# Kernel optimization log

Hardware: AMD Instinct MI355X
Metric: run time of the kernel (lower is better)

## Reference

```python
import jax, jax.numpy as jnp
import numpy as np
from jax import lax

SEQ, B, F, L = 32, 32, 64, 256
OC = 128          # out_channels
K = 5
PAD = (K - 1) // 2
GROUPS = 4 * OC // 32  # GroupNorm groups = 16
EPS = 1e-5


def group_norm(x, w, b):
    # x: (B, C, L); normalize over each group's (C//G, L) slice
    bsz, c, l = x.shape
    xg = x.reshape(bsz, GROUPS, -1)
    mu = jnp.mean(xg, axis=-1, keepdims=True)
    var = jnp.var(xg, axis=-1, keepdims=True)
    xg = (xg - mu) * lax.rsqrt(var + EPS)
    return xg.reshape(bsz, c, l) * w[None, :, None] + b[None, :, None]


def setup_inputs() -> dict:
    key = jax.random.key(0)
    k1, k2, k3 = jax.random.split(key, 3)
    fan_in = (F + OC) * K
    return {
        "inputs": jax.random.normal(k1, (SEQ, B, F, L), dtype=jnp.float32),
        "conv_w": jax.random.normal(k2, (4 * OC, F + OC, K), dtype=jnp.float32) / np.sqrt(fan_in),
        "conv_b": jax.random.normal(k3, (4 * OC,), dtype=jnp.float32) * 0.01,
        "gn_w": jnp.ones((4 * OC,), dtype=jnp.float32),
        "gn_b": jnp.zeros((4 * OC,), dtype=jnp.float32),
    }


def reference(inputs, conv_w, conv_b, gn_w, gn_b):
    bsz, sub_len = inputs.shape[1], inputs.shape[3]
    hx0 = jnp.zeros((bsz, OC, sub_len), dtype=inputs.dtype)
    cx0 = jnp.zeros((bsz, OC, sub_len), dtype=inputs.dtype)

    def step(carry, x):
        hx, cx = carry
        combined = jnp.concatenate([x, hx], axis=1)  # (B, F+OC, L)
        gates = lax.conv_general_dilated(
            combined, conv_w, window_strides=(1,), padding=[(PAD, PAD)],
            dimension_numbers=("NCH", "OIH", "NCH"))
        gates = gates + conv_b[None, :, None]
        gates = group_norm(gates, gn_w, gn_b)
        i, f, g, o = jnp.split(gates, 4, axis=1)
        cy = jax.nn.sigmoid(f) * cx + jax.nn.sigmoid(i) * jnp.tanh(g)
        hy = jax.nn.sigmoid(o) * jnp.tanh(cy)
        return (hy, cy), hy

    (hy, cy), outputs = lax.scan(step, (hx0, cx0), inputs)
    return outputs, (hy, cy)
```

## Files before the change

### kernel.cpp

```cpp
#include <hip/hip_runtime.h>

typedef unsigned short u16;
typedef unsigned int u32;
typedef unsigned long long u64;
typedef __attribute__((ext_vector_type(4))) float f32x4;
typedef __attribute__((ext_vector_type(8))) short s16x8;
typedef __attribute__((ext_vector_type(4))) int i32x4;

#define EPS 1e-5f

__device__ __forceinline__ u16 f2bf(float f) {
  unsigned u = __float_as_uint(f);
  return (u16)((u + 0x7fffu + ((u >> 16) & 1u)) >> 16);
}
__device__ __forceinline__ float sigm(float x) { return 1.0f / (1.0f + __expf(-x)); }
__device__ __forceinline__ float tanh_f(float x) {
  float e = __expf(-2.0f * fabsf(x));
  float r = (1.0f - e) / (1.0f + e);
  return copysignf(r, x);
}
__device__ __forceinline__ void gl_lds16(const void* g, void* l) {
  __builtin_amdgcn_global_load_lds(
      (const __attribute__((address_space(1))) u32*)g,
      (__attribute__((address_space(3))) u32*)l, 16, 0, 0);
}

__global__ __launch_bounds__(256) void k_setup(
    const float* __restrict__ cw, u16* __restrict__ Wpk,
    const float* __restrict__ x, u16* __restrict__ xT,
    i32x4* __restrict__ hTz, i32x4* __restrict__ cxz, i32x4* __restrict__ flz) {
  const int bid = blockIdx.x, tid = threadIdx.x;
  __shared__ __align__(16) u16 ltile[256 * 72];
  if (bid < 1920) {
    int idx = bid * 256 + tid;
    int f = idx >> 9, r = idx & 511;
    int lane = r >> 3, j = r & 7;
    int of = f & 31, tk = f >> 5;
    int kk = tk % 6, tap = tk / 6;
    int o = (of << 4) + (lane & 15);
    int c = (kk << 5) + ((lane >> 4) << 3) + j;
    Wpk[idx] = f2bf(cw[(o * 192 + c) * 5 + tap]);
  } else if (bid < 2944) {
    int tb = bid - 1920;
    const float* src = x + tb * (64 * 256);
    for (int it = 0; it < 64; ++it) {
      int idx = it * 256 + tid;
      int c = idx >> 8, l = idx & 255;
      ltile[l * 72 + c] = f2bf(src[idx]);
    }
    __syncthreads();
    char* dst = (char*)(xT + tb * 16896);
    i32x4 z = {0, 0, 0, 0};
    for (int i = tid; i < 2112; i += 256) {
      int r = i >> 3, ch = i & 7;
      i32x4 v = z;
      if (r >= 2 && r < 258) v = *(const i32x4*)(ltile + (r - 2) * 72 + ch * 8);
      *(i32x4*)(dst + r * 128 + ((ch * 16) ^ ((r & 7) << 4))) = v;
    }
  } else {
    int base = (bid - 2944) * 256 + tid;
    i32x4 z = {0, 0, 0, 0};
    for (int i = base; i < 270336; i += 131072) hTz[i] = z;
    for (int i = base; i < 262144; i += 131072) cxz[i] = z;
    for (int i = base; i < 2048;   i += 131072) flz[i] = z;
  }
}

__global__ __launch_bounds__(512) void k_step(
    const u16* __restrict__ Wpk, const u16* __restrict__ xT, u16* __restrict__ hT,
    const float* __restrict__ cb, const float* __restrict__ gnw, const float* __restrict__ gnb,
    float* __restrict__ cx, float* __restrict__ out,
    float* __restrict__ stats, int* __restrict__ flags, int t) {
  const int bid = blockIdx.x;
  const int b = bid & 31, lh = (bid >> 5) & 1, cs = bid >> 6;
  const int L0 = lh << 7;
  const int tid = threadIdx.x, wave = tid >> 6, lane = tid & 63;
  const int wm = wave & 1, wl = wave >> 1;
  const int l15 = lane & 15, q = lane >> 4;
  const int cgrp = q << 4;

  __shared__ __align__(16) char ldsx[16896];
  __shared__ __align__(16) char ldsh[33792];
  __shared__ __align__(16) char hl[8192];
  __shared__ float red[8][4][2];
  __shared__ float blkstat[8];
  __shared__ float smu[4], srs[4];

  const u16* hTr = hT + (t & 1) * 1081344;
  u16* hTw = hT + ((t + 1) & 1) * 1081344;

  {
    const char* gx = (const char*)(xT + ((t << 5) + b) * 16896) + (lh << 14);
    for (int i = tid; i < 1056; i += 512) gl_lds16(gx + (i << 4), ldsx + (i << 4));
  }
  __builtin_amdgcn_sched_barrier(0);
  {
    const char* gh = (const char*)hTr + b * 67584 + (lh << 15);
    for (int i = tid; i < 2112; i += 512) gl_lds16(gh + (i << 4), ldsh + (i << 4));
  }
  __builtin_amdgcn_sched_barrier(0);
  asm volatile("s_waitcnt vmcnt(4)" ::: "memory");
  __builtin_amdgcn_s_barrier();
  __builtin_amdgcn_sched_barrier(0);

  f32x4 zero4 = {0.f, 0.f, 0.f, 0.f};
  f32x4 acc[4][2];
  #pragma unroll
  for (int g = 0; g < 4; ++g) { acc[g][0] = zero4; acc[g][1] = zero4; }

  const s16x8* Wv = (const s16x8*)Wpk;

  #pragma unroll
  for (int tap = 0; tap < 5; ++tap) {
    #pragma unroll
    for (int kk = 0; kk < 2; ++kk) {
      const int cc = tap * 6 + kk;
      s16x8 av[4], bv[2];
      #pragma unroll
      for (int g = 0; g < 4; ++g) {
        const int of = (g << 3) + (cs << 1) + wm;
        av[g] = Wv[(((cc << 5) + of) << 6) + lane];
      }
      #pragma unroll
      for (int ni = 0; ni < 2; ++ni) {
        const int rr = (wl << 5) + (ni << 4) + l15 + tap;
        const int sw = (rr & 7) << 4;
        bv[ni] = *(const s16x8*)(ldsx + (rr << 7) + (((kk << 6) + cgrp) ^ sw));
      }
      #pragma unroll
      for (int g = 0; g < 4; ++g) {
        acc[g][0] = __builtin_amdgcn_mfma_f32_16x16x32_bf16(av[g], bv[0], acc[g][0], 0, 0, 0);
        acc[g][1] = __builtin_amdgcn_mfma_f32_16x16x32_bf16(av[g], bv[1], acc[g][1], 0, 0, 0);
      }
    }
  }
  __builtin_amdgcn_sched_barrier(0);
  asm volatile("s_waitcnt vmcnt(0)" ::: "memory");
  __builtin_amdgcn_s_barrier();
  __builtin_amdgcn_sched_barrier(0);

  #pragma unroll
  for (int tap = 0; tap < 5; ++tap) {
    #pragma unroll
    for (int kk2 = 0; kk2 < 4; ++kk2) {
      const int cc = tap * 6 + kk2 + 2;
      s16x8 av[4], bv[2];
      #pragma unroll
      for (int g = 0; g < 4; ++g) {
        const int of = (g << 3) + (cs << 1) + wm;
        av[g] = Wv[(((cc << 5) + of) << 6) + lane];
      }
      #pragma unroll
      for (int ni = 0; ni < 2; ++ni) {
        const int rr = (wl << 5) + (ni << 4) + l15 + tap;
        const int sw = (rr & 7) << 4;
        bv[ni] = *(const s16x8*)(ldsh + (rr << 8) + (((kk2 << 6) + cgrp) ^ sw));
      }
      #pragma unroll
      for (int g = 0; g < 4; ++g) {
        acc[g][0] = __builtin_amdgcn_mfma_f32_16x16x32_bf16(av[g], bv[0], acc[g][0], 0, 0, 0);
        acc[g][1] = __builtin_amdgcn_mfma_f32_16x16x32_bf16(av[g], bv[1], acc[g][1], 0, 0, 0);
      }
    }
  }

  const int chq = (cs << 5) + (wm << 4) + (q << 2);
  float sum4[4], sq4[4];
  #pragma unroll
  for (int g = 0; g < 4; ++g) {
    const f32x4 bias = *(const f32x4*)(cb + (g << 7) + chq);
    sum4[g] = 0.f; sq4[g] = 0.f;
    #pragma unroll
    for (int ni = 0; ni < 2; ++ni)
      #pragma unroll
      for (int r = 0; r < 4; ++r) {
        float v = acc[g][ni][r] + bias[r];
        acc[g][ni][r] = v;
        sum4[g] += v; sq4[g] += v * v;
      }
  }
  f32x4 w4[4], b4[4];
  float cxv[2][4];
  #pragma unroll
  for (int g = 0; g < 4; ++g) {
    w4[g] = *(const f32x4*)(gnw + (g << 7) + chq);
    b4[g] = *(const f32x4*)(gnb + (g << 7) + chq);
  }
  #pragma unroll
  for (int ni = 0; ni < 2; ++ni) {
    const int l = L0 + (wl << 5) + (ni << 4) + l15;
    #pragma unroll
    for (int r = 0; r < 4; ++r)
      cxv[ni][r] = cx[(b << 15) + ((chq + r) << 8) + l];
  }
  #pragma unroll
  for (int off = 1; off < 64; off <<= 1) {
    #pragma unroll
    for (int g = 0; g < 4; ++g) {
      sum4[g] += __shfl_xor(sum4[g], off);
      sq4[g]  += __shfl_xor(sq4[g], off);
    }
  }
  if (lane == 0) {
    #pragma unroll
    for (int g = 0; g < 4; ++g) { red[wave][g][0] = sum4[g]; red[wave][g][1] = sq4[g]; }
  }
  __syncthreads();
  if (tid < 8) {
    const int g = tid >> 1, j = tid & 1;
    float v = 0.f;
    #pragma unroll
    for (int w = 0; w < 8; ++w) v += red[w][g][j];
    blkstat[tid] = v;
  }
  __syncthreads();

  const int sidx = (((t << 5) + b) << 3) + (cs << 1) + lh;
  if (tid == 0) {
    float* sp = stats + (sidx << 3);
    #pragma unroll
    for (int j = 0; j < 8; ++j)
      __hip_atomic_store(sp + j, blkstat[j], __ATOMIC_RELAXED, __HIP_MEMORY_SCOPE_AGENT);
    __hip_atomic_store(&flags[sidx], 1, __ATOMIC_RELEASE, __HIP_MEMORY_SCOPE_AGENT);
    while (__hip_atomic_load(&flags[sidx ^ 1], __ATOMIC_RELAXED, __HIP_MEMORY_SCOPE_AGENT) == 0)
      __builtin_amdgcn_s_sleep(2);
    __builtin_amdgcn_fence(__ATOMIC_ACQUIRE, "agent");
    const float* pe = stats + ((sidx & ~1) << 3);
    const float* po = stats + ((sidx | 1) << 3);
    const float inv = 1.0f / 8192.0f;
    #pragma unroll
    for (int g = 0; g < 4; ++g) {
      float s = __hip_atomic_load(pe + (g << 1), __ATOMIC_RELAXED, __HIP_MEMORY_SCOPE_AGENT)
              + __hip_atomic_load(po + (g << 1), __ATOMIC_RELAXED, __HIP_MEMORY_SCOPE_AGENT);
      float qv = __hip_atomic_load(pe + (g << 1) + 1, __ATOMIC_RELAXED, __HIP_MEMORY_SCOPE_AGENT)
               + __hip_atomic_load(po + (g << 1) + 1, __ATOMIC_RELAXED, __HIP_MEMORY_SCOPE_AGENT);
      float m = s * inv;
      smu[g] = m;
      srs[g] = rsqrtf(qv * inv - m * m + EPS);
    }
  }
  __syncthreads();

  const float mu0 = smu[0], mu1 = smu[1], mu2 = smu[2], mu3 = smu[3];
  const float rs0 = srs[0], rs1 = srs[1], rs2 = srs[2], rs3 = srs[3];
  float* outp = out + (((t << 5) + b) << 15);
  #pragma unroll
  for (int ni = 0; ni < 2; ++ni) {
    const int l = L0 + (wl << 5) + (ni << 4) + l15;
    const int ll = l - L0;
    u16 hp[4];
    #pragma unroll
    for (int r = 0; r < 4; ++r) {
      const int c = chq + r;
      float vi = (acc[0][ni][r] - mu0) * rs0 * w4[0][r] + b4[0][r];
      float vf = (acc[1][ni][r] - mu1) * rs1 * w4[1][r] + b4[1][r];
      float vg = (acc[2][ni][r] - mu2) * rs2 * w4[2][r] + b4[2][r];
      float vo = (acc[3][ni][r] - mu3) * rs3 * w4[3][r] + b4[3][r];
      float cyv = sigm(vf) * cxv[ni][r] + sigm(vi) * tanh_f(vg);
      float hyv = sigm(vo) * tanh_f(cyv);
      const int ci = (c << 8) + l;
      cx[(b << 15) + ci] = cyv;
      outp[ci] = hyv;
      hp[r] = f2bf(hyv);
      if (t == 31) {
        out[33554432 + (b << 15) + ci] = hyv;
        out[34603008 + (b << 15) + ci] = cyv;
      }
    }
    *(u64*)(hl + (ll << 6) + (((wm << 5) + (q << 3)) ^ ((ll & 3) << 4))) =
        *(const u64*)hp;
  }
  __syncthreads();

  {
    const int ll = tid >> 2, k = tid & 3;
    const int row = L0 + ll + 2;
    i32x4 v = *(const i32x4*)(hl + (ll << 6) + ((k << 4) ^ ((ll & 3) << 4)));
    char* dst = (char*)hTw + b * 67584 + (row << 8) +
                ((((cs << 2) + k) << 4) ^ ((row & 7) << 4));
    *(i32x4*)dst = v;
  }
}

extern "C" void kernel_launch(void* const* d_in, const int* in_sizes, int n_in,
                              void* d_out, int out_size, void* d_ws, size_t ws_size,
                              hipStream_t stream) {
  const float* x  = (const float*)d_in[0];
  const float* cw = (const float*)d_in[1];
  const float* cb = (const float*)d_in[2];
  const float* gw = (const float*)d_in[3];
  const float* gb = (const float*)d_in[4];
  float* out = (float*)d_out;
  char* ws = (char*)d_ws;

  u16*   Wpk   = (u16*)(ws);
  u16*   xT    = (u16*)(ws + 983040);
  u16*   hT    = (u16*)(ws + 35586048);
  float* cx    = (float*)(ws + 39911424);
  float* stats = (float*)(ws + 44105728);
  int*   flags = (int*)(ws + 44367872);

  k_setup<<<3456, 256, 0, stream>>>(cw, Wpk, x, xT, (i32x4*)hT, (i32x4*)cx, (i32x4*)flags);
  for (int t = 0; t < 32; ++t)
    k_step<<<256, 512, 0, stream>>>(Wpk, xT, hT, cb, gw, gb, cx, out, stats, flags, t);
}
```

Baseline: 665.4 us.

## Split step kernel into 512 blocks of 256 threads with four-way stat exchange

Each step kernel now runs 512 blocks of 256 threads, with each block handling a quarter of the sequence length instead of a half. This fills more of the CUs on the device and lets two blocks share a CU, at the cost of more halo reload and more cross-block GroupNorm synchronisation. The stats exchange is reworked so that eight threads store partial sums directly and three lanes each spin on one of three peer flags. Four lanes then combine the group stats. The flag buffer is moved and enlarged to fit the bigger grid.

Measured after the change: 738.2 us. 1.11x slower.

```diff
diff --git a/kernel.cpp b/kernel.cpp
--- a/kernel.cpp
+++ b/kernel.cpp
@@ -62,41 +62,40 @@
     i32x4 z = {0, 0, 0, 0};
     for (int i = base; i < 270336; i += 131072) hTz[i] = z;
     for (int i = base; i < 262144; i += 131072) cxz[i] = z;
-    for (int i = base; i < 2048;   i += 131072) flz[i] = z;
-  }
-}
-
-__global__ __launch_bounds__(512) void k_step(
+    if (base < 4096) flz[base] = z;
+  }
+}
+
+__global__ __launch_bounds__(256, 2) void k_step(
     const u16* __restrict__ Wpk, const u16* __restrict__ xT, u16* __restrict__ hT,
     const float* __restrict__ cb, const float* __restrict__ gnw, const float* __restrict__ gnb,
     float* __restrict__ cx, float* __restrict__ out,
     float* __restrict__ stats, int* __restrict__ flags, int t) {
   const int bid = blockIdx.x;
-  const int b = bid & 31, lh = (bid >> 5) & 1, cs = bid >> 6;
-  const int L0 = lh << 7;
+  const int b = bid & 31, lq = (bid >> 5) & 3, cs = bid >> 7;
+  const int L0 = lq << 6;
   const int tid = threadIdx.x, wave = tid >> 6, lane = tid & 63;
   const int wm = wave & 1, wl = wave >> 1;
   const int l15 = lane & 15, q = lane >> 4;
   const int cgrp = q << 4;
 
-  __shared__ __align__(16) char ldsx[16896];
-  __shared__ __align__(16) char ldsh[33792];
-  __shared__ __align__(16) char hl[8192];
-  __shared__ float red[8][4][2];
-  __shared__ float blkstat[8];
+  __shared__ __align__(16) char ldsx[8704];
+  __shared__ __align__(16) char ldsh[17408];
+  __shared__ __align__(16) char hl[4096];
+  __shared__ float red[4][4][2];
   __shared__ float smu[4], srs[4];
 
   const u16* hTr = hT + (t & 1) * 1081344;
   u16* hTw = hT + ((t + 1) & 1) * 1081344;
 
   {
-    const char* gx = (const char*)(xT + ((t << 5) + b) * 16896) + (lh << 14);
-    for (int i = tid; i < 1056; i += 512) gl_lds16(gx + (i << 4), ldsx + (i << 4));
+    const char* gx = (const char*)(xT + ((t << 5) + b) * 16896) + (lq << 13);
+    for (int i = tid; i < 544; i += 256) gl_lds16(gx + (i << 4), ldsx + (i << 4));
   }
   __builtin_amdgcn_sched_barrier(0);
   {
-    const char* gh = (const char*)hTr + b * 67584 + (lh << 15);
-    for (int i = tid; i < 2112; i += 512) gl_lds16(gh + (i << 4), ldsh + (i << 4));
+    const char* gh = (const char*)hTr + b * 67584 + (lq << 14);
+    for (int i = tid; i < 1088; i += 256) gl_lds16(gh + (i << 4), ldsh + (i << 4));
   }
   __builtin_amdgcn_sched_barrier(0);
   asm volatile("s_waitcnt vmcnt(4)" ::: "memory");
@@ -206,37 +205,37 @@
     for (int g = 0; g < 4; ++g) { red[wave][g][0] = sum4[g]; red[wave][g][1] = sq4[g]; }
   }
   __syncthreads();
+
+  const int gbase = ((((t << 5) + b) << 2) + cs) << 2;
+  const int sidx = gbase | lq;
   if (tid < 8) {
     const int g = tid >> 1, j = tid & 1;
-    float v = 0.f;
-    #pragma unroll
-    for (int w = 0; w < 8; ++w) v += red[w][g][j];
-    blkstat[tid] = v;
-  }
-  __syncthreads();
-
-  const int sidx = (((t << 5) + b) << 3) + (cs << 1) + lh;
-  if (tid == 0) {
-    float* sp = stats + (sidx << 3);
-    #pragma unroll
-    for (int j = 0; j < 8; ++j)
-      __hip_atomic_store(sp + j, blkstat[j], __ATOMIC_RELAXED, __HIP_MEMORY_SCOPE_AGENT);
-    __hip_atomic_store(&flags[sidx], 1, __ATOMIC_RELEASE, __HIP_MEMORY_SCOPE_AGENT);
-    while (__hip_atomic_load(&flags[sidx ^ 1], __ATOMIC_RELAXED, __HIP_MEMORY_SCOPE_AGENT) == 0)
-      __builtin_amdgcn_s_sleep(2);
-    __builtin_amdgcn_fence(__ATOMIC_ACQUIRE, "agent");
-    const float* pe = stats + ((sidx & ~1) << 3);
-    const float* po = stats + ((sidx | 1) << 3);
-    const float inv = 1.0f / 8192.0f;
-    #pragma unroll
-    for (int g = 0; g < 4; ++g) {
-      float s = __hip_atomic_load(pe + (g << 1), __ATOMIC_RELAXED, __HIP_MEMORY_SCOPE_AGENT)
-              + __hip_atomic_load(po + (g << 1), __ATOMIC_RELAXED, __HIP_MEMORY_SCOPE_AGENT);
-      float qv = __hip_atomic_load(pe + (g << 1) + 1, __ATOMIC_RELAXED, __HIP_MEMORY_SCOPE_AGENT)
-               + __hip_atomic_load(po + (g << 1) + 1, __ATOMIC_RELAXED, __HIP_MEMORY_SCOPE_AGENT);
+    float v = red[0][g][j] + red[1][g][j] + red[2][g][j] + red[3][g][j];
+    __hip_atomic_store(stats + (sidx << 3) + tid, v, __ATOMIC_RELAXED, __HIP_MEMORY_SCOPE_AGENT);
+  }
+  if (wave == 0) {
+    asm volatile("s_waitcnt vmcnt(0)" ::: "memory");
+    if (tid == 0)
+      __hip_atomic_store(&flags[sidx], 1, __ATOMIC_RELEASE, __HIP_MEMORY_SCOPE_AGENT);
+    if (tid < 3) {
+      const int p = tid + (tid >= lq ? 1 : 0);
+      while (__hip_atomic_load(&flags[gbase | p], __ATOMIC_RELAXED, __HIP_MEMORY_SCOPE_AGENT) == 0)
+        __builtin_amdgcn_s_sleep(2);
+    }
+    if (tid < 4) {
+      __builtin_amdgcn_fence(__ATOMIC_ACQUIRE, "agent");
+      float s = 0.f, qv = 0.f;
+      #pragma unroll
+      for (int p = 0; p < 4; ++p) {
+        s  += __hip_atomic_load(stats + ((gbase | p) << 3) + (tid << 1),
+                                __ATOMIC_RELAXED, __HIP_MEMORY_SCOPE_AGENT);
+        qv += __hip_atomic_load(stats + ((gbase | p) << 3) + (tid << 1) + 1,
+                                __ATOMIC_RELAXED, __HIP_MEMORY_SCOPE_AGENT);
+      }
+      const float inv = 1.0f / 8192.0f;
       float m = s * inv;
-      smu[g] = m;
-      srs[g] = rsqrtf(qv * inv - m * m + EPS);
+      smu[tid] = m;
+      srs[tid] = rsqrtf(qv * inv - m * m + EPS);
     }
   }
   __syncthreads();
@@ -298,9 +297,9 @@
   u16*   hT    = (u16*)(ws + 35586048);
   float* cx    = (float*)(ws + 39911424);
   float* stats = (float*)(ws + 44105728);
-  int*   flags = (int*)(ws + 44367872);
+  int*   flags = (int*)(ws + 44630016);
 
   k_setup<<<3456, 256, 0, stream>>>(cw, Wpk, x, xT, (i32x4*)hT, (i32x4*)cx, (i32x4*)flags);
   for (int t = 0; t < 32; ++t)
-    k_step<<<256, 512, 0, stream>>>(Wpk, xT, hT, cb, gw, gb, cx, out, stats, flags, t);
-}
+    k_step<<<512, 256, 0, stream>>>(Wpk, xT, hT, cb, gw, gb, cx, out, stats, flags, t);
+}
```

## Fuse two LSTM timesteps per launch with a per-batch inter-block flag barrier

Applied to the files above, without the earlier changes.

Each launch now runs two consecutive timesteps. Between them, the 8 blocks that share a batch element synchronize through epoch flags in global memory, then reload the new hidden state. This halves the number of kernel launches and their launch and drain overhead, and the next step's x tile is prefetched before the barrier. It relies on all 256 blocks being co-resident so the spin-waits cannot deadlock, and it adds an extra flag region that must be zeroed at setup.

New measurement: 1.561 ms. 135% more time.

```diff
diff --git a/kernel.cpp b/kernel.cpp
--- a/kernel.cpp
+++ b/kernel.cpp
@@ -62,15 +62,15 @@
     i32x4 z = {0, 0, 0, 0};
     for (int i = base; i < 270336; i += 131072) hTz[i] = z;
     for (int i = base; i < 262144; i += 131072) cxz[i] = z;
-    for (int i = base; i < 2048;   i += 131072) flz[i] = z;
+    for (int i = base; i < 3072;   i += 131072) flz[i] = z;
   }
 }
 
-__global__ __launch_bounds__(512) void k_step(
+__global__ __launch_bounds__(512, 1) void k_step2(
     const u16* __restrict__ Wpk, const u16* __restrict__ xT, u16* __restrict__ hT,
     const float* __restrict__ cb, const float* __restrict__ gnw, const float* __restrict__ gnb,
     float* __restrict__ cx, float* __restrict__ out,
-    float* __restrict__ stats, int* __restrict__ flags, int t) {
+    float* __restrict__ stats, int* __restrict__ flags, int* __restrict__ flags2, int t0) {
   const int bid = blockIdx.x;
   const int b = bid & 31, lh = (bid >> 5) & 1, cs = bid >> 6;
   const int L0 = lh << 7;
@@ -81,21 +81,17 @@
 
   __shared__ __align__(16) char ldsx[16896];
   __shared__ __align__(16) char ldsh[33792];
-  __shared__ __align__(16) char hl[8192];
+  __shared__ __align__(16) char hl[32768];
   __shared__ float red[8][4][2];
-  __shared__ float blkstat[8];
   __shared__ float smu[4], srs[4];
 
-  const u16* hTr = hT + (t & 1) * 1081344;
-  u16* hTw = hT + ((t + 1) & 1) * 1081344;
-
   {
-    const char* gx = (const char*)(xT + ((t << 5) + b) * 16896) + (lh << 14);
+    const char* gx = (const char*)(xT + ((t0 << 5) + b) * 16896) + (lh << 14);
     for (int i = tid; i < 1056; i += 512) gl_lds16(gx + (i << 4), ldsx + (i << 4));
   }
   __builtin_amdgcn_sched_barrier(0);
   {
-    const char* gh = (const char*)hTr + b * 67584 + (lh << 15);
+    const char* gh = (const char*)(hT + (t0 & 1) * 1081344) + b * 67584 + (lh << 15);
     for (int i = tid; i < 2112; i += 512) gl_lds16(gh + (i << 4), ldsh + (i << 4));
   }
   __builtin_amdgcn_sched_barrier(0);
@@ -103,182 +99,214 @@
   __builtin_amdgcn_s_barrier();
   __builtin_amdgcn_sched_barrier(0);
 
-  f32x4 zero4 = {0.f, 0.f, 0.f, 0.f};
-  f32x4 acc[4][2];
+  const s16x8* Wv = (const s16x8*)Wpk;
+
   #pragma unroll
-  for (int g = 0; g < 4; ++g) { acc[g][0] = zero4; acc[g][1] = zero4; }
-
-  const s16x8* Wv = (const s16x8*)Wpk;
-
-  #pragma unroll
-  for (int tap = 0; tap < 5; ++tap) {
-    #pragma unroll
-    for (int kk = 0; kk < 2; ++kk) {
-      const int cc = tap * 6 + kk;
-      s16x8 av[4], bv[2];
+  for (int s = 0; s < 2; ++s) {
+    const int t = t0 + s;
+    u16* hTw = hT + ((t + 1) & 1) * 1081344;
+
+    f32x4 zero4 = {0.f, 0.f, 0.f, 0.f};
+    f32x4 acc[4][2];
+    #pragma unroll
+    for (int g = 0; g < 4; ++g) { acc[g][0] = zero4; acc[g][1] = zero4; }
+
+    #pragma unroll
+    for (int tap = 0; tap < 5; ++tap) {
+      #pragma unroll
+      for (int kk = 0; kk < 2; ++kk) {
+        const int cc = tap * 6 + kk;
+        s16x8 av[4], bv[2];
+        #pragma unroll
+        for (int g = 0; g < 4; ++g) {
+          const int of = (g << 3) + (cs << 1) + wm;
+          av[g] = Wv[(((cc << 5) + of) << 6) + lane];
+        }
+        #pragma unroll
+        for (int ni = 0; ni < 2; ++ni) {
+          const int rr = (wl << 5) + (ni << 4) + l15 + tap;
+          const int sw = (rr & 7) << 4;
+          bv[ni] = *(const s16x8*)(ldsx + (rr << 7) + (((kk << 6) + cgrp) ^ sw));
+        }
+        #pragma unroll
+        for (int g = 0; g < 4; ++g) {
+          acc[g][0] = __builtin_amdgcn_mfma_f32_16x16x32_bf16(av[g], bv[0], acc[g][0], 0, 0, 0);
+          acc[g][1] = __builtin_amdgcn_mfma_f32_16x16x32_bf16(av[g], bv[1], acc[g][1], 0, 0, 0);
+        }
+      }
+    }
+    __builtin_amdgcn_sched_barrier(0);
+    asm volatile("s_waitcnt vmcnt(0)" ::: "memory");
+    __builtin_amdgcn_s_barrier();
+    __builtin_amdgcn_sched_barrier(0);
+
+    #pragma unroll
+    for (int tap = 0; tap < 5; ++tap) {
+      #pragma unroll
+      for (int kk2 = 0; kk2 < 4; ++kk2) {
+        const int cc = tap * 6 + kk2 + 2;
+        s16x8 av[4], bv[2];
+        #pragma unroll
+        for (int g = 0; g < 4; ++g) {
+          const int of = (g << 3) + (cs << 1) + wm;
+          av[g] = Wv[(((cc << 5) + of) << 6) + lane];
+        }
+        #pragma unroll
+        for (int ni = 0; ni < 2; ++ni) {
+          const int rr = (wl << 5) + (ni << 4) + l15 + tap;
+          const int sw = (rr & 7) << 4;
+          bv[ni] = *(const s16x8*)(ldsh + (rr << 8) + (((kk2 << 6) + cgrp) ^ sw));
+        }
+        #pragma unroll
+        for (int g = 0; g < 4; ++g) {
+          acc[g][0] = __builtin_amdgcn_mfma_f32_16x16x32_bf16(av[g], bv[0], acc[g][0], 0, 0, 0);
+          acc[g][1] = __builtin_amdgcn_mfma_f32_16x16x32_bf16(av[g], bv[1], acc[g][1], 0, 0, 0);
+        }
+      }
+    }
+
+    const int chq = (cs << 5) + (wm << 4) + (q << 2);
+    float sum4[4], sq4[4];
+    #pragma unroll
+    for (int g = 0; g < 4; ++g) {
+      const f32x4 bias = *(const f32x4*)(cb + (g << 7) + chq);
+      sum4[g] = 0.f; sq4[g] = 0.f;
+      #pragma unroll
+      for (int ni = 0; ni < 2; ++ni)
+        #pragma unroll
+        for (int r = 0; r < 4; ++r) {
+          float v = acc[g][ni][r] + bias[r];
+          acc[g][ni][r] = v;
+          sum4[g] += v; sq4[g] += v * v;
+        }
+    }
+    f32x4 w4[4], b4[4];
+    float cxv[2][4];
+    #pragma unroll
+    for (int g = 0; g < 4; ++g) {
+      w4[g] = *(const f32x4*)(gnw + (g << 7) + chq);
+      b4[g] = *(const f32x4*)(gnb + (g << 7) + chq);
+    }
+    #pragma unroll
+    for (int ni = 0; ni < 2; ++ni) {
+      const int l = L0 + (wl << 5) + (ni << 4) + l15;
+      #pragma unroll
+      for (int r = 0; r < 4; ++r)
+        cxv[ni][r] = cx[(b << 15) + ((chq + r) << 8) + l];
+    }
+    #pragma unroll
+    for (int off = 1; off < 64; off <<= 1) {
       #pragma unroll
       for (int g = 0; g < 4; ++g) {
-        const int of = (g << 3) + (cs << 1) + wm;
-        av[g] = Wv[(((cc << 5) + of) << 6) + lane];
-      }
-      #pragma unroll
-      for (int ni = 0; ni < 2; ++ni) {
-        const int rr = (wl << 5) + (ni << 4) + l15 + tap;
-        const int sw = (rr & 7) << 4;
-        bv[ni] = *(const s16x8*)(ldsx + (rr << 7) + (((kk << 6) + cgrp) ^ sw));
-      }
+        sum4[g] += __shfl_xor(sum4[g], off);
+        sq4[g]  += __shfl_xor(sq4[g], off);
+      }
+    }
+    if (lane == 0) {
+      #pragma unroll
+      for (int g = 0; g < 4; ++g) { red[wave][g][0] = sum4[g]; red[wave][g][1] = sq4[g]; }
+    }
+    __syncthreads();
+
+    const int sidx = (((t << 5) + b) << 3) + (cs << 1) + lh;
+    if (tid == 0) {
+      float* sp = stats + (sidx << 3);
       #pragma unroll
       for (int g = 0; g < 4; ++g) {
-        acc[g][0] = __builtin_amdgcn_mfma_f32_16x16x32_bf16(av[g], bv[0], acc[g][0], 0, 0, 0);
-        acc[g][1] = __builtin_amdgcn_mfma_f32_16x16x32_bf16(av[g], bv[1], acc[g][1], 0, 0, 0);
-      }
-    }
-  }
-  __builtin_amdgcn_sched_barrier(0);
-  asm volatile("s_waitcnt vmcnt(0)" ::: "memory");
-  __builtin_amdgcn_s_barrier();
-  __builtin_amdgcn_sched_barrier(0);
-
-  #pragma unroll
-  for (int tap = 0; tap < 5; ++tap) {
-    #pragma unroll
-    for (int kk2 = 0; kk2 < 4; ++kk2) {
-      const int cc = tap * 6 + kk2 + 2;
-      s16x8 av[4], bv[2];
+        float sv = 0.f, qv = 0.f;
+        #pragma unroll
+        for (int w = 0; w < 8; ++w) { sv += red[w][g][0]; qv += red[w][g][1]; }
+        __hip_atomic_store(sp + (g << 1),     sv, __ATOMIC_RELAXED, __HIP_MEMORY_SCOPE_AGENT);
+        __hip_atomic_store(sp + (g << 1) + 1, qv, __ATOMIC_RELAXED, __HIP_MEMORY_SCOPE_AGENT);
+      }
+      __hip_atomic_store(&flags[sidx], 1, __ATOMIC_RELEASE, __HIP_MEMORY_SCOPE_AGENT);
+      while (__hip_atomic_load(&flags[sidx ^ 1], __ATOMIC_RELAXED, __HIP_MEMORY_SCOPE_AGENT) == 0)
+        __builtin_amdgcn_s_sleep(2);
+      __builtin_amdgcn_fence(__ATOMIC_ACQUIRE, "agent");
+      const float* pe = stats + ((sidx & ~1) << 3);
+      const float* po = stats + ((sidx | 1) << 3);
+      const float inv = 1.0f / 8192.0f;
       #pragma unroll
       for (int g = 0; g < 4; ++g) {
-        const int of = (g << 3) + (cs << 1) + wm;
-        av[g] = Wv[(((cc << 5) + of) << 6) + lane];
-      }
-      #pragma unroll
-      for (int ni = 0; ni < 2; ++ni) {
-        const int rr = (wl << 5) + (ni << 4) + l15 + tap;
-        const int sw = (rr & 7) << 4;
-        bv[ni] = *(const s16x8*)(ldsh + (rr << 8) + (((kk2 << 6) + cgrp) ^ sw));
-      }
-      #pragma unroll
-      for (int g = 0; g < 4; ++g) {
-        acc[g][0] = __builtin_amdgcn_mfma_f32_16x16x32_bf16(av[g], bv[0], acc[g][0], 0, 0, 0);
-        acc[g][1] = __builtin_amdgcn_mfma_f32_16x16x32_bf16(av[g], bv[1], acc[g][1], 0, 0, 0);
-      }
-    }
-  }
-
-  const int chq = (cs << 5) + (wm << 4) + (q << 2);
-  float sum4[4], sq4[4];
-  #pragma unroll
-  for (int g = 0; g < 4; ++g) {
-    const f32x4 bias = *(const f32x4*)(cb + (g << 7) + chq);
-    sum4[g] = 0.f; sq4[g] = 0.f;
-    #pragma unroll
-    for (int ni = 0; ni < 2; ++ni)
+        float sv = __hip_atomic_load(pe + (g << 1), __ATOMIC_RELAXED, __HIP_MEMORY_SCOPE_AGENT)
+                 + __hip_atomic_load(po + (g << 1), __ATOMIC_RELAXED, __HIP_MEMORY_SCOPE_AGENT);
+        float qv = __hip_atomic_load(pe + (g << 1) + 1, __ATOMIC_RELAXED, __HIP_MEMORY_SCOPE_AGENT)
+                 + __hip_atomic_load(po + (g << 1) + 1, __ATOMIC_RELAXED, __HIP_MEMORY_SCOPE_AGENT);
+        float m = sv * inv;
+        smu[g] = m;
+        srs[g] = rsqrtf(qv * inv - m * m + EPS);
+      }
+    }
+    __syncthreads();
+
+    const float mu0 = smu[0], mu1 = smu[1], mu2 = smu[2], mu3 = smu[3];
+    const float rs0 = srs[0], rs1 = srs[1], rs2 = srs[2], rs3 = srs[3];
+    float* outp = out + (((t << 5) + b) << 15);
+    #pragma unroll
+    for (int ni = 0; ni < 2; ++ni) {
+      const int l = L0 + (wl << 5) + (ni << 4) + l15;
+      const int ll = l - L0;
+      u16 hp[4];
       #pragma unroll
       for (int r = 0; r < 4; ++r) {
-        float v = acc[g][ni][r] + bias[r];
-        acc[g][ni][r] = v;
-        sum4[g] += v; sq4[g] += v * v;
-      }
-  }
-  f32x4 w4[4], b4[4];
-  float cxv[2][4];
-  #pragma unroll
-  for (int g = 0; g < 4; ++g) {
-    w4[g] = *(const f32x4*)(gnw + (g << 7) + chq);
-    b4[g] = *(const f32x4*)(gnb + (g << 7) + chq);
-  }
-  #pragma unroll
-  for (int ni = 0; ni < 2; ++ni) {
-    const int l = L0 + (wl << 5) + (ni << 4) + l15;
-    #pragma unroll
-    for (int r = 0; r < 4; ++r)
-      cxv[ni][r] = cx[(b << 15) + ((chq + r) << 8) + l];
-  }
-  #pragma unroll
-  for (int off = 1; off < 64; off <<= 1) {
-    #pragma unroll
-    for (int g = 0; g < 4; ++g) {
-      sum4[g] += __shfl_xor(sum4[g], off);
-      sq4[g]  += __shfl_xor(sq4[g], off);
-    }
-  }
-  if (lane == 0) {
-    #pragma unroll
-    for (int g = 0; g < 4; ++g) { red[wave][g][0] = sum4[g]; red[wave][g][1] = sq4[g]; }
-  }
-  __syncthreads();
-  if (tid < 8) {
-    const int g = tid >> 1, j = tid & 1;
-    float v = 0.f;
-    #pragma unroll
-    for (int w = 0; w < 8; ++w) v += red[w][g][j];
-    blkstat[tid] = v;
-  }
-  __syncthreads();
-
-  const int sidx = (((t << 5) + b) << 3) + (cs << 1) + lh;
-  if (tid == 0) {
-    float* sp = stats + (sidx << 3);
-    #pragma unroll
-    for (int j = 0; j < 8; ++j)
-      __hip_atomic_store(sp + j, blkstat[j], __ATOMIC_RELAXED, __HIP_MEMORY_SCOPE_AGENT);
-    __hip_atomic_store(&flags[sidx], 1, __ATOMIC_RELEASE, __HIP_MEMORY_SCOPE_AGENT);
-    while (__hip_atomic_load(&flags[sidx ^ 1], __ATOMIC_RELAXED, __HIP_MEMORY_SCOPE_AGENT) == 0)
-      __builtin_amdgcn_s_sleep(2);
-    __builtin_amdgcn_fence(__ATOMIC_ACQUIRE, "agent");
-    const float* pe = stats + ((sidx & ~1) << 3);
-    const float* po = stats + ((sidx | 1) << 3);
-    const float inv = 1.0f / 8192.0f;
-    #pragma unroll
-    for (int g = 0; g < 4; ++g) {
-      float s = __hip_atomic_load(pe + (g << 1), __ATOMIC_RELAXED, __HIP_MEMORY_SCOPE_AGENT)
-              + __hip_atomic_load(po + (g << 1), __ATOMIC_RELAXED, __HIP_MEMORY_SCOPE_AGENT);
-      float qv = __hip_atomic_load(pe + (g << 1) + 1, __ATOMIC_RELAXED, __HIP_MEMORY_SCOPE_AGENT)
-               + __hip_atomic_load(po + (g << 1) + 1, __ATOMIC_RELAXED, __HIP_MEMORY_SCOPE_AGENT);
-      float m = s * inv;
-      smu[g] = m;
-      srs[g] = rsqrtf(qv * inv - m * m + EPS);
-    }
-  }
-  __syncthreads();
-
-  const float mu0 = smu[0], mu1 = smu[1], mu2 = smu[2], mu3 = smu[3];
-  const float rs0 = srs[0], rs1 = srs[1], rs2 = srs[2], rs3 = srs[3];
-  float* outp = out + (((t << 5) + b) << 15);
-  #pragma unroll
-  for (int ni = 0; ni < 2; ++ni) {
-    const int l = L0 + (wl << 5) + (ni << 4) + l15;
-    const int ll = l - L0;
-    u16 hp[4];
-    #pragma unroll
-    for (int r = 0; r < 4; ++r) {
-      const int c = chq + r;
-      float vi = (acc[0][ni][r] - mu0) * rs0 * w4[0][r] + b4[0][r];
-      float vf = (acc[1][ni][r] - mu1) * rs1 * w4[1][r] + b4[1][r];
-      float vg = (acc[2][ni][r] - mu2) * rs2 * w4[2][r] + b4[2][r];
-      float vo = (acc[3][ni][r] - mu3) * rs3 * w4[3][r] + b4[3][r];
-      float cyv = sigm(vf) * cxv[ni][r] + sigm(vi) * tanh_f(vg);
-      float hyv = sigm(vo) * tanh_f(cyv);
-      const int ci = (c << 8) + l;
-      cx[(b << 15) + ci] = cyv;
-      outp[ci] = hyv;
-      hp[r] = f2bf(hyv);
-      if (t == 31) {
-        out[33554432 + (b << 15) + ci] = hyv;
-        out[34603008 + (b << 15) + ci] = cyv;
-      }
-    }
-    *(u64*)(hl + (ll << 6) + (((wm << 5) + (q << 3)) ^ ((ll & 3) << 4))) =
-        *(const u64*)hp;
-  }
-  __syncthreads();
-
-  {
-    const int ll = tid >> 2, k = tid & 3;
-    const int row = L0 + ll + 2;
-    i32x4 v = *(const i32x4*)(hl + (ll << 6) + ((k << 4) ^ ((ll & 3) << 4)));
-    char* dst = (char*)hTw + b * 67584 + (row << 8) +
-                ((((cs << 2) + k) << 4) ^ ((row & 7) << 4));
-    *(i32x4*)dst = v;
+        const int c = chq + r;
+        float vi = (acc[0][ni][r] - mu0) * rs0 * w4[0][r] + b4[0][r];
+        float vf = (acc[1][ni][r] - mu1) * rs1 * w4[1][r] + b4[1][r];
+        float vg = (acc[2][ni][r] - mu2) * rs2 * w4[2][r] + b4[2][r];
+        float vo = (acc[3][ni][r] - mu3) * rs3 * w4[3][r] + b4[3][r];
+        float cyv = sigm(vf) * cxv[ni][r] + sigm(vi) * tanh_f(vg);
+        float hyv = sigm(vo) * tanh_f(cyv);
+        const int ci = (c << 8) + l;
+        cx[(b << 15) + ci] = cyv;
+        outp[ci] = hyv;
+        hp[r] = f2bf(hyv);
+        if (t == 31) {
+          out[33554432 + (b << 15) + ci] = hyv;
+          out[34603008 + (b << 15) + ci] = cyv;
+        }
+      }
+      *(u64*)(hl + (ll << 6) + (((wm << 5) + (q << 3)) ^ ((ll & 3) << 4))) =
+          *(const u64*)hp;
+    }
+    __syncthreads();
+
+    {
+      const int ll = tid >> 2, k = tid & 3;
+      const int row = L0 + ll + 2;
+      i32x4 v = *(const i32x4*)(hl + (ll << 6) + ((k << 4) ^ ((ll & 3) << 4)));
+      char* dst = (char*)hTw + b * 67584 + (row << 8) +
+                  ((((cs << 2) + k) << 4) ^ ((row & 7) << 4));
+      *(i32x4*)dst = v;
+    }
+
+    if (s == 0) {
+      {
+        const char* gx = (const char*)(xT + (((t + 1) << 5) + b) * 16896) + (lh << 14);
+        for (int i = tid; i < 1056; i += 512) gl_lds16(gx + (i << 4), ldsx + (i << 4));
+      }
+      asm volatile("s_waitcnt vmcnt(0)" ::: "memory");
+      __syncthreads();
+      const int ep = (t0 >> 1) + 1;
+      if (tid == 0) {
+        __builtin_amdgcn_fence(__ATOMIC_RELEASE, "agent");
+        __hip_atomic_store(flags2 + (bid << 4), ep, __ATOMIC_RELAXED, __HIP_MEMORY_SCOPE_AGENT);
+      }
+      if (tid < 8) {
+        const int pb = (tid << 5) | b;
+        if (pb != bid) {
+          while (__hip_atomic_load(flags2 + (pb << 4), __ATOMIC_RELAXED, __HIP_MEMORY_SCOPE_AGENT) < ep)
+            __builtin_amdgcn_s_sleep(2);
+        }
+      }
+      __syncthreads();
+      if (tid == 0) __builtin_amdgcn_fence(__ATOMIC_ACQUIRE, "agent");
+      __syncthreads();
+      {
+        const char* gh = (const char*)(hT + ((t + 1) & 1) * 1081344) + b * 67584 + (lh << 15);
+        for (int i = tid; i < 2112; i += 512) gl_lds16(gh + (i << 4), ldsh + (i << 4));
+      }
+      __builtin_amdgcn_sched_barrier(0);
+    }
   }
 }
 
@@ -293,14 +321,15 @@
   float* out = (float*)d_out;
   char* ws = (char*)d_ws;
 
-  u16*   Wpk   = (u16*)(ws);
-  u16*   xT    = (u16*)(ws + 983040);
-  u16*   hT    = (u16*)(ws + 35586048);
-  float* cx    = (float*)(ws + 39911424);
-  float* stats = (float*)(ws + 44105728);
-  int*   flags = (int*)(ws + 44367872);
+  u16*   Wpk    = (u16*)(ws);
+  u16*   xT     = (u16*)(ws + 983040);
+  u16*   hT     = (u16*)(ws + 35586048);
+  float* cx     = (float*)(ws + 39911424);
+  float* stats  = (float*)(ws + 44105728);
+  int*   flags  = (int*)(ws + 44367872);
+  int*   flags2 = (int*)(ws + 44400640);
 
   k_setup<<<3456, 256, 0, stream>>>(cw, Wpk, x, xT, (i32x4*)hT, (i32x4*)cx, (i32x4*)flags);
-  for (int t = 0; t < 32; ++t)
-    k_step<<<256, 512, 0, stream>>>(Wpk, xT, hT, cb, gw, gb, cx, out, stats, flags, t);
-}
+  for (int t0 = 0; t0 < 32; t0 += 2)
+    k_step2<<<256, 512, 0, stream>>>(Wpk, xT, hT, cb, gw, gb, cx, out, stats, flags, flags2, t0);
+}
```
